# Kernel tuning notes

Hardware: AMD Instinct MI355X
Metric: run time of the kernel (lower is better)

## Reference

```python
import jax, jax.numpy as jnp
import numpy as np

NUM_NEIGHBORS = (10, 25)  # FLAGS.num_neighbors = '10_25'
MAX_DEGREE = 64
L = 2  # num encoder layers


def _sample(nodes, neighbors_out, neighbors_in, key):
    """Multi-hop uniform neighbor sampling (shuffle columns + slice, as in TF code)."""
    samples = [nodes]
    support = 1
    supports = [1]
    for k in range(L):
        t = L - 1 - k
        n = NUM_NEIGHBORS[t]
        support *= 2 * n
        supports.append(support)
        key, k1, k2 = jax.random.split(key, 3)
        # tf.transpose(tf.random.shuffle(tf.transpose(x))) shuffles neighbor slots
        # with ONE permutation shared across all rows, then slices first n.
        cols_out = jax.random.permutation(k1, MAX_DEGREE)[:n]
        cols_in = jax.random.permutation(k2, MAX_DEGREE)[:n]
        nout = neighbors_out[samples[k]][:, cols_out]  # [prev, n]
        nin = neighbors_in[samples[k]][:, cols_in]     # [prev, n]
        samples.append(jnp.concatenate([nout, nin], axis=1).reshape(-1))
    return samples, supports


def _gc(self_v, nei_out, nei_in, W):
    # GraphConvolution: mean-aggregate out/in neighbors, concat with self, linear, sigmoid.
    agg = jnp.concatenate([self_v, nei_out.mean(axis=1), nei_in.mean(axis=1)], axis=-1)
    return jax.nn.sigmoid(agg @ W)


def _aggregate(inputs, supports, layer, W, B):
    h_hop = []
    for hop in range(L - layer):
        n = NUM_NEIGHBORS[L - hop - 1]
        nei = inputs[hop + 1].reshape(B * supports[hop], 2 * n, -1)
        self_v = inputs[hop].reshape(B * supports[hop], -1)
        h_hop.append(_gc(self_v, nei[:, :n], nei[:, n:], W))
    return h_hop


def _forward(nodes1, nodes2, neighbors_out, neighbors_in, features,
             W_in, W_mean, W_std, W_pi, W_ag, W_ad, Wd_mean, Wd_std, Wd_pi):
    B = nodes1.shape[0]
    key = jax.random.key(42)
    k1, k2 = jax.random.split(key)
    s1, sup1 = _sample(nodes1, neighbors_out, neighbors_in, k1)
    s2, sup2 = _sample(nodes2, neighbors_out, neighbors_in, k2)
    in1 = [features[s] for s in s1]  # hop-wise gathered features
    in2 = [features[s] for s in s2]
    # layer 0: shared input GC
    h1 = _aggregate(in1, sup1, 0, W_in, B)
    h2 = _aggregate(in2, sup2, 0, W_in, B)
    # layer 1: parameter heads (mean/std/pi/alpha)
    h_mean1 = _aggregate(h1, sup1, 1, W_mean, B)[0]
    h_mean2 = _aggregate(h2, sup2, 1, W_mean, B)[0]
    h_std1 = _aggregate(h1, sup1, 1, W_std, B)[0]
    h_std2 = _aggregate(h2, sup2, 1, W_std, B)[0]
    h_pi1 = _aggregate(h1, sup1, 1, W_pi, B)[0]
    h_pi2 = _aggregate(h2, sup2, 1, W_pi, B)[0]
    # final fully-connected projections (act = identity)
    z_mean1 = h_mean1 @ Wd_mean
    z_mean2 = h_mean2 @ Wd_mean
    z_std1 = h_std1 @ Wd_std
    z_std2 = h_std2 @ Wd_std
    pi_logit1 = h_pi1 @ Wd_pi
    pi_logit2 = h_pi2 @ Wd_pi
    return jnp.stack([z_mean1, z_std1, pi_logit1, z_mean2, z_std2, pi_logit2])


def setup_inputs() -> dict:
    key = jax.random.key(0)
    ks = jax.random.split(key, 16)
    N, F, B = 200000, 128, 256
    E, D = 128, 64
    inp = {
        'nodes1': jax.random.randint(ks[0], (B,), 0, N, dtype=jnp.int32),
        'nodes2': jax.random.randint(ks[1], (B,), 0, N, dtype=jnp.int32),
        'neighbors_out': jax.random.randint(ks[2], (N, MAX_DEGREE), 0, N, dtype=jnp.int32),
        'neighbors_in': jax.random.randint(ks[3], (N, MAX_DEGREE), 0, N, dtype=jnp.int32),
        'features': jax.random.normal(ks[4], (N, F), dtype=jnp.float32),
        'W_in': jax.random.normal(ks[5], (3 * F, E), dtype=jnp.float32) * 0.05,
        'W_mean': jax.random.normal(ks[6], (3 * E, E), dtype=jnp.float32) * 0.05,
        'W_std': jax.random.normal(ks[7], (3 * E, E), dtype=jnp.float32) * 0.05,
        'W_pi': jax.random.normal(ks[8], (3 * E, E), dtype=jnp.float32) * 0.05,
        'W_ag': jax.random.normal(ks[9], (3 * E, E), dtype=jnp.float32) * 0.05,
        'W_ad': jax.random.normal(ks[10], (3 * E, E), dtype=jnp.float32) * 0.05,
        'Wd_mean': jax.random.normal(ks[11], (E, D), dtype=jnp.float32) * 0.05,
        'Wd_std': jax.random.normal(ks[12], (E, D), dtype=jnp.float32) * 0.05,
        'Wd_pi': jax.random.normal(ks[13], (E, D), dtype=jnp.float32) * 0.05,
    }
    return inp


def reference(nodes1, nodes2, neighbors_out, neighbors_in, features,
              W_in, W_mean, W_std, W_pi, W_ag, W_ad, Wd_mean, Wd_std, Wd_pi):
    return _forward(nodes1, nodes2, neighbors_out, neighbors_in, features,
                    W_in, W_mean, W_std, W_pi, W_ag, W_ad, Wd_mean, Wd_std, Wd_pi)
```

## Files before the change

kernel.cpp:

```cpp
#include <hip/hip_runtime.h>
#include <stdint.h>
#include <math.h>

#define FDIM 128
#define KDIM 384
#define NROWS 26112

struct Cols { int o25[25]; int i25[25]; int o10[10]; int i10[10]; };
struct ColsBoth { Cols c[2]; };

static inline uint32_t rotl32(uint32_t x, uint32_t r){ return (x<<r)|(x>>(32u-r)); }

static void tf2x32(uint32_t k0, uint32_t k1, uint32_t c0, uint32_t c1,
                   uint32_t& o0, uint32_t& o1){
  const uint32_t ra[4] = {13u,15u,26u,6u};
  const uint32_t rb[4] = {17u,29u,16u,24u};
  uint32_t ks2 = k0 ^ k1 ^ 0x1BD11BDAu;
  uint32_t x0 = c0 + k0, x1 = c1 + k1;
  for(int i=0;i<4;i++){ x0 += x1; x1 = rotl32(x1, ra[i]); x1 ^= x0; }
  x0 += k1; x1 += ks2 + 1u;
  for(int i=0;i<4;i++){ x0 += x1; x1 = rotl32(x1, rb[i]); x1 ^= x0; }
  x0 += ks2; x1 += k0 + 2u;
  for(int i=0;i<4;i++){ x0 += x1; x1 = rotl32(x1, ra[i]); x1 ^= x0; }
  x0 += k0; x1 += k1 + 3u;
  for(int i=0;i<4;i++){ x0 += x1; x1 = rotl32(x1, rb[i]); x1 ^= x0; }
  x0 += k1; x1 += ks2 + 4u;
  for(int i=0;i<4;i++){ x0 += x1; x1 = rotl32(x1, ra[i]); x1 ^= x0; }
  x0 += ks2; x1 += k0 + 5u;
  o0 = x0; o1 = x1;
}

static void jax_split_child(uint32_t ka, uint32_t kb, uint32_t i,
                            uint32_t& oa, uint32_t& ob){
  tf2x32(ka, kb, 0u, i, oa, ob);
}

static uint32_t jax_bits32(uint32_t ka, uint32_t kb, uint32_t i){
  uint32_t a,b; tf2x32(ka, kb, 0u, i, a, b);
  return a ^ b;
}

static void jax_perm64(uint32_t ka, uint32_t kb, int* perm){
  uint32_t sa, sb; jax_split_child(ka, kb, 1u, sa, sb);
  uint32_t b[64]; int v[64];
  for(int i=0;i<64;i++){ b[i]=jax_bits32(sa, sb, (uint32_t)i); v[i]=i; }
  for(int i=1;i<64;i++){
    uint32_t bb=b[i]; int vv=v[i]; int j=i-1;
    while(j>=0 && b[j]>bb){ b[j+1]=b[j]; v[j+1]=v[j]; j--; }
    b[j+1]=bb; v[j+1]=vv;
  }
  for(int i=0;i<64;i++) perm[i]=v[i];
}

static void compute_cols(ColsBoth& cb){
  uint32_t k1a,k1b,k2a,k2b;
  jax_split_child(0u, 42u, 0u, k1a, k1b);
  jax_split_child(0u, 42u, 1u, k2a, k2b);
  for(int side=0; side<2; side++){
    uint32_t ka = side ? k2a : k1a;
    uint32_t kb = side ? k2b : k1b;
    uint32_t nka,nkb, c1a,c1b, c2a,c2b;
    jax_split_child(ka,kb,0u,nka,nkb);
    jax_split_child(ka,kb,1u,c1a,c1b);
    jax_split_child(ka,kb,2u,c2a,c2b);
    int p[64];
    jax_perm64(c1a,c1b,p); for(int i=0;i<25;i++) cb.c[side].o25[i]=p[i];
    jax_perm64(c2a,c2b,p); for(int i=0;i<25;i++) cb.c[side].i25[i]=p[i];
    uint32_t d1a,d1b,d2a,d2b;
    jax_split_child(nka,nkb,1u,d1a,d1b);
    jax_split_child(nka,nkb,2u,d2a,d2b);
    jax_perm64(d1a,d1b,p); for(int i=0;i<10;i++) cb.c[side].o10[i]=p[i];
    jax_perm64(d2a,d2b,p); for(int i=0;i<10;i++) cb.c[side].i10[i]=p[i];
  }
}

__device__ __forceinline__ float getc(const float4& v, int i){
  return (i==0)?v.x:(i==1)?v.y:(i==2)?v.z:v.w;
}
__device__ __forceinline__ float sigf(float x){ return 1.0f/(1.0f+expf(-x)); }
__device__ __forceinline__ void add4(float4& s, const float4& v){
  s.x+=v.x; s.y+=v.y; s.z+=v.z; s.w+=v.w;
}


__global__ __launch_bounds__(256) void gather_kernel(
    const float* __restrict__ feat,
    const int* __restrict__ nodes1, const int* __restrict__ nodes2,
    const int* __restrict__ nout, const int* __restrict__ nin,
    float* __restrict__ agg, int base_row, ColsBoth cb)
{
  int t = threadIdx.x;
  int row_local = blockIdx.x*8 + (t>>5);
  int lane = t & 31;
  int c0 = lane*4;
  int row = base_row + row_local;

  float4 selfv, so, si;

  if(row < 512){
    int side = row >> 8, b = row & 255;
    int node = (side ? nodes2 : nodes1)[b];
    const Cols& c = cb.c[side];
    const long nb = (long)node*64;
    selfv = *(const float4*)(feat + (long)node*FDIM + c0);
    int ido[25], idi[25];
    #pragma unroll
    for(int i=0;i<25;i++) ido[i] = nout[nb + c.o25[i]];
    #pragma unroll
    for(int i=0;i<25;i++) idi[i] = nin[nb + c.i25[i]];
    float4 acco = make_float4(0,0,0,0);
    float4 acci = make_float4(0,0,0,0);
    #pragma unroll
    for(int jj=0; jj<25; jj+=5){
      float4 vo[5], vi[5];
      #pragma unroll
      for(int i=0;i<5;i++) vo[i] = *(const float4*)(feat + (long)ido[jj+i]*FDIM + c0);
      #pragma unroll
      for(int i=0;i<5;i++) vi[i] = *(const float4*)(feat + (long)idi[jj+i]*FDIM + c0);
      #pragma unroll
      for(int i=0;i<5;i++) add4(acco, vo[i]);
      #pragma unroll
      for(int i=0;i<5;i++) add4(acci, vi[i]);
    }
    so = make_float4(acco.x/25.f, acco.y/25.f, acco.z/25.f, acco.w/25.f);
    si = make_float4(acci.x/25.f, acci.y/25.f, acci.z/25.f, acci.w/25.f);
  } else {
    int hrow = row - 512;
    int side = (hrow >= 12800) ? 1 : 0;
    int r = side ? (hrow - 12800) : hrow;
    int b = r / 50, slot = r % 50;
    const Cols& c = cb.c[side];
    int root = (side ? nodes2 : nodes1)[b];
    int node;
    if(slot < 25) node = nout[(long)root*64 + c.o25[slot]];
    else          node = nin [(long)root*64 + c.i25[slot-25]];
    const long nb = (long)node*64;
    selfv = *(const float4*)(feat + (long)node*FDIM + c0);
    int oid[10], iid[10];
    #pragma unroll
    for(int j=0;j<10;j++) oid[j] = nout[nb + c.o10[j]];
    #pragma unroll
    for(int j=0;j<10;j++) iid[j] = nin[nb + c.i10[j]];
    float4 acco = make_float4(0,0,0,0);
    float4 acci = make_float4(0,0,0,0);
    #pragma unroll
    for(int jj=0; jj<10; jj+=5){
      float4 vo[5], vi[5];
      #pragma unroll
      for(int j=0;j<5;j++) vo[j] = *(const float4*)(feat + (long)oid[jj+j]*FDIM + c0);
      #pragma unroll
      for(int j=0;j<5;j++) vi[j] = *(const float4*)(feat + (long)iid[jj+j]*FDIM + c0);
      #pragma unroll
      for(int j=0;j<5;j++) add4(acco, vo[j]);
      #pragma unroll
      for(int j=0;j<5;j++) add4(acci, vi[j]);
    }
    so = make_float4(acco.x*0.1f, acco.y*0.1f, acco.z*0.1f, acco.w*0.1f);
    si = make_float4(acci.x*0.1f, acci.y*0.1f, acci.z*0.1f, acci.w*0.1f);
  }

  float* ar = agg + (long)row_local*KDIM;
  *(float4*)(ar + c0)       = selfv;
  *(float4*)(ar + 128 + c0) = so;
  *(float4*)(ar + 256 + c0) = si;
}

__global__ __launch_bounds__(256) void gemm_sig_kernel(
    const float* __restrict__ A, const float* __restrict__ W,
    float* __restrict__ out)
{
  __shared__ float Wbuf[96*128];
  int t = threadIdx.x, lane = t&15, rg = t>>4;
  int r0 = blockIdx.x*64 + rg*4;
  int c0 = lane*8;
  float acc[4][8];
  #pragma unroll
  for(int r=0;r<4;r++)
    #pragma unroll
    for(int i=0;i<8;i++) acc[r][i]=0.f;

  for(int kc=0; kc<4; kc++){
    __syncthreads();
    const float4* ws = (const float4*)(W + kc*96*128);
    float4* wd = (float4*)Wbuf;
    #pragma unroll
    for(int i=0;i<12;i++) wd[i*256+t] = ws[i*256+t];
    __syncthreads();
    const float* Ab = A + (long)r0*KDIM + kc*96;
    #pragma unroll 2
    for(int k4=0;k4<96;k4+=4){
      float4 a0 = *(const float4*)(Ab + 0*KDIM + k4);
      float4 a1 = *(const float4*)(Ab + 1*KDIM + k4);
      float4 a2 = *(const float4*)(Ab + 2*KDIM + k4);
      float4 a3 = *(const float4*)(Ab + 3*KDIM + k4);
      #pragma unroll
      for(int kk=0;kk<4;kk++){
        float av0=getc(a0,kk), av1=getc(a1,kk), av2=getc(a2,kk), av3=getc(a3,kk);
        const float* wr = Wbuf + (k4+kk)*128 + c0;
        float4 w0 = *(const float4*)wr;
        float4 w1 = *(const float4*)(wr+4);
        acc[0][0]+=av0*w0.x; acc[0][1]+=av0*w0.y; acc[0][2]+=av0*w0.z; acc[0][3]+=av0*w0.w;
        acc[0][4]+=av0*w1.x; acc[0][5]+=av0*w1.y; acc[0][6]+=av0*w1.z; acc[0][7]+=av0*w1.w;
        acc[1][0]+=av1*w0.x; acc[1][1]+=av1*w0.y; acc[1][2]+=av1*w0.z; acc[1][3]+=av1*w0.w;
        acc[1][4]+=av1*w1.x; acc[1][5]+=av1*w1.y; acc[1][6]+=av1*w1.z; acc[1][7]+=av1*w1.w;
        acc[2][0]+=av2*w0.x; acc[2][1]+=av2*w0.y; acc[2][2]+=av2*w0.z; acc[2][3]+=av2*w0.w;
        acc[2][4]+=av2*w1.x; acc[2][5]+=av2*w1.y; acc[2][6]+=av2*w1.z; acc[2][7]+=av2*w1.w;
        acc[3][0]+=av3*w0.x; acc[3][1]+=av3*w0.y; acc[3][2]+=av3*w0.z; acc[3][3]+=av3*w0.w;
        acc[3][4]+=av3*w1.x; acc[3][5]+=av3*w1.y; acc[3][6]+=av3*w1.z; acc[3][7]+=av3*w1.w;
      }
    }
  }
  #pragma unroll
  for(int r=0;r<4;r++){
    float4 o0, o1;
    o0.x=sigf(acc[r][0]); o0.y=sigf(acc[r][1]); o0.z=sigf(acc[r][2]); o0.w=sigf(acc[r][3]);
    o1.x=sigf(acc[r][4]); o1.y=sigf(acc[r][5]); o1.z=sigf(acc[r][6]); o1.w=sigf(acc[r][7]);
    float* op = out + (long)(r0+r)*FDIM + c0;
    *(float4*)op = o0; *(float4*)(op+4) = o1;
  }
}

__global__ __launch_bounds__(256) void head_kernel(
    const float* __restrict__ h,
    const float* __restrict__ Wm, const float* __restrict__ Ws, const float* __restrict__ Wp,
    const float* __restrict__ Dm, const float* __restrict__ Ds, const float* __restrict__ Dp,
    float* __restrict__ out)
{
  __shared__ float As[KDIM];
  __shared__ float Ps[4*FDIM];
  __shared__ float Hs[FDIM];
  __shared__ float Qs[4*64];
  int head = blockIdx.x >> 9;
  int grow = blockIdx.x & 511;
  int t = threadIdx.x;
  const float* W = (head==0) ? Wm : (head==1) ? Ws : Wp;
  const float* D = (head==0) ? Dm : (head==1) ? Ds : Dp;

  {
    int c = t & 127;
    int half = t >> 7;
    const float* nb = h + (long)(512 + grow*50 + half*25)*FDIM + c;
    float s = 0.f;
    #pragma unroll
    for(int jj=0;jj<25;jj+=5){
      float v0 = nb[(long)(jj+0)*FDIM];
      float v1 = nb[(long)(jj+1)*FDIM];
      float v2 = nb[(long)(jj+2)*FDIM];
      float v3 = nb[(long)(jj+3)*FDIM];
      float v4 = nb[(long)(jj+4)*FDIM];
      s += v0+v1+v2+v3+v4;
    }
    As[128 + half*128 + c] = s/25.f;
    if(half==0) As[c] = h[(long)grow*FDIM + c];
  }
  __syncthreads();

  {
    int c2 = (t & 63)*2;
    int kq = t >> 6;
    const float* wp = W + (long)(kq*96)*FDIM + c2;
    const float* as = As + kq*96;
    float a0=0.f, a1=0.f;
    #pragma unroll 8
    for(int k=0;k<96;k++){
      float a = as[k];
      float2 w = *(const float2*)(wp + (long)k*FDIM);
      a0 += a*w.x; a1 += a*w.y;
    }
    Ps[kq*FDIM + c2]   = a0;
    Ps[kq*FDIM + c2+1] = a1;
  }
  __syncthreads();
  if(t < 64){
    int c2 = t*2;
    float s0 = Ps[c2]     + Ps[FDIM+c2]     + Ps[2*FDIM+c2]     + Ps[3*FDIM+c2];
    float s1 = Ps[c2+1]   + Ps[FDIM+c2+1]   + Ps[2*FDIM+c2+1]   + Ps[3*FDIM+c2+1];
    Hs[c2]   = sigf(s0);
    Hs[c2+1] = sigf(s1);
  }
  __syncthreads();

  {
    int col = t & 63;
    int kq = t >> 6;
    const float* dp = D + (long)(kq*32)*64 + col;
    const float* hs = Hs + kq*32;
    float a = 0.f;
    #pragma unroll 8
    for(int k=0;k<32;k++){
      a += hs[k] * dp[(long)k*64];
    }
    Qs[kq*64 + col] = a;
  }
  __syncthreads();
  if(t < 64){
    float a = Qs[t] + Qs[64+t] + Qs[128+t] + Qs[192+t];
    int side = grow >> 8, b = grow & 255;
    out[((long)(side*3+head)*256 + b)*64 + t] = a;
  }
}

extern "C" void kernel_launch(void* const* d_in, const int* in_sizes, int n_in,
                              void* d_out, int out_size, void* d_ws, size_t ws_size,
                              hipStream_t stream) {
  const int*   nodes1  = (const int*)d_in[0];
  const int*   nodes2  = (const int*)d_in[1];
  const int*   nout    = (const int*)d_in[2];
  const int*   nin     = (const int*)d_in[3];
  const float* feat    = (const float*)d_in[4];
  const float* W_in    = (const float*)d_in[5];
  const float* W_mean  = (const float*)d_in[6];
  const float* W_std   = (const float*)d_in[7];
  const float* W_pi    = (const float*)d_in[8];
  const float* Wd_mean = (const float*)d_in[11];
  const float* Wd_std  = (const float*)d_in[12];
  const float* Wd_pi   = (const float*)d_in[13];
  float* out = (float*)d_out;

  float* h    = (float*)d_ws;
  float* aggC = h + (size_t)NROWS*FDIM;

  size_t fixedB = (size_t)NROWS*FDIM*4;
  const int ncOpt[5] = {1,2,4,12,51};
  int nc = 51;
  for(int i=0;i<5;i++){
    size_t need = fixedB + ((size_t)NROWS/ncOpt[i])*KDIM*4;
    if(need <= ws_size){ nc = ncOpt[i]; break; }
  }
  int chunkRows = NROWS / nc;

  ColsBoth cb;
  compute_cols(cb);

  for(int c=0;c<nc;c++){
    int base = c*chunkRows;
    gather_kernel<<<chunkRows/8, 256, 0, stream>>>(feat, nodes1, nodes2,
                                                   nout, nin, aggC, base, cb);
    gemm_sig_kernel<<<chunkRows/64, 256, 0, stream>>>(aggC, W_in, h + (size_t)base*FDIM);
  }
  head_kernel<<<1536, 256, 0, stream>>>(h, W_mean, W_std, W_pi, Wd_mean, Wd_std, Wd_pi, out);
}
```

Measured before the change: 313.6 us.

## Fuse neighbor gather and input GEMM into one kernel via shared memory

The gather kernel now writes its 32-row aggregate tile into shared memory, and the same block runs the W_in GEMM with sigmoid on that tile. This removes the global round trip of the aggregated 384-wide rows and the chunked launch loop. In exchange, each block streams the full W_in through shared memory for only 32 rows, so weight traffic per row rises. The larger shared-memory footprint (about 74 KB) may also reduce occupancy while the gather is latency-bound.

Result: slower. 321.5 us (+2.5%).

```diff
diff --git a/kernel.cpp b/kernel.cpp
--- a/kernel.cpp
+++ b/kernel.cpp
@@ -5,6 +5,9 @@
 #define FDIM 128
 #define KDIM 384
 #define NROWS 26112
+#define ASTRIDE 388
+#define BROWS 32
+#define KCH 48
 
 struct Cols { int o25[25]; int i25[25]; int o10[10]; int i10[10]; };
 struct ColsBoth { Cols c[2]; };
@@ -83,140 +86,139 @@
 }
 
 
-__global__ __launch_bounds__(256) void gather_kernel(
+__global__ __launch_bounds__(256) void fused_gg_kernel(
     const float* __restrict__ feat,
     const int* __restrict__ nodes1, const int* __restrict__ nodes2,
     const int* __restrict__ nout, const int* __restrict__ nin,
-    float* __restrict__ agg, int base_row, ColsBoth cb)
+    const float* __restrict__ W,
+    float* __restrict__ h, ColsBoth cb)
 {
+  __shared__ float As[BROWS*ASTRIDE];
+  __shared__ float Wbuf[KCH*FDIM];
   int t = threadIdx.x;
-  int row_local = blockIdx.x*8 + (t>>5);
-  int lane = t & 31;
-  int c0 = lane*4;
-  int row = base_row + row_local;
-
-  float4 selfv, so, si;
-
-  if(row < 512){
-    int side = row >> 8, b = row & 255;
-    int node = (side ? nodes2 : nodes1)[b];
-    const Cols& c = cb.c[side];
-    const long nb = (long)node*64;
-    selfv = *(const float4*)(feat + (long)node*FDIM + c0);
-    int ido[25], idi[25];
+
+  {
+    int g = t >> 5;
+    int lane = t & 31;
+    int c0 = lane*4;
+    #pragma unroll 1
+    for(int rr=0; rr<4; rr++){
+      int lrow = rr*8 + g;
+      int row = blockIdx.x*BROWS + lrow;
+      float4 selfv, so, si;
+
+      if(row < 512){
+        int side = row >> 8, b = row & 255;
+        int node = (side ? nodes2 : nodes1)[b];
+        const Cols& c = cb.c[side];
+        const long nb = (long)node*64;
+        selfv = *(const float4*)(feat + (long)node*FDIM + c0);
+        int ido[25], idi[25];
+        #pragma unroll
+        for(int i=0;i<25;i++) ido[i] = nout[nb + c.o25[i]];
+        #pragma unroll
+        for(int i=0;i<25;i++) idi[i] = nin[nb + c.i25[i]];
+        float4 acco = make_float4(0,0,0,0);
+        float4 acci = make_float4(0,0,0,0);
+        #pragma unroll
+        for(int jj=0; jj<25; jj+=5){
+          float4 vo[5], vi[5];
+          #pragma unroll
+          for(int i=0;i<5;i++) vo[i] = *(const float4*)(feat + (long)ido[jj+i]*FDIM + c0);
+          #pragma unroll
+          for(int i=0;i<5;i++) vi[i] = *(const float4*)(feat + (long)idi[jj+i]*FDIM + c0);
+          #pragma unroll
+          for(int i=0;i<5;i++) add4(acco, vo[i]);
+          #pragma unroll
+          for(int i=0;i<5;i++) add4(acci, vi[i]);
+        }
+        so = make_float4(acco.x/25.f, acco.y/25.f, acco.z/25.f, acco.w/25.f);
+        si = make_float4(acci.x/25.f, acci.y/25.f, acci.z/25.f, acci.w/25.f);
+      } else {
+        int hrow = row - 512;
+        int side = (hrow >= 12800) ? 1 : 0;
+        int r = side ? (hrow - 12800) : hrow;
+        int b = r / 50, slot = r % 50;
+        const Cols& c = cb.c[side];
+        int root = (side ? nodes2 : nodes1)[b];
+        int node;
+        if(slot < 25) node = nout[(long)root*64 + c.o25[slot]];
+        else          node = nin [(long)root*64 + c.i25[slot-25]];
+        const long nb = (long)node*64;
+        selfv = *(const float4*)(feat + (long)node*FDIM + c0);
+        int oid[10], iid[10];
+        #pragma unroll
+        for(int j=0;j<10;j++) oid[j] = nout[nb + c.o10[j]];
+        #pragma unroll
+        for(int j=0;j<10;j++) iid[j] = nin[nb + c.i10[j]];
+        float4 acco = make_float4(0,0,0,0);
+        float4 acci = make_float4(0,0,0,0);
+        #pragma unroll
+        for(int jj=0; jj<10; jj+=5){
+          float4 vo[5], vi[5];
+          #pragma unroll
+          for(int j=0;j<5;j++) vo[j] = *(const float4*)(feat + (long)oid[jj+j]*FDIM + c0);
+          #pragma unroll
+          for(int j=0;j<5;j++) vi[j] = *(const float4*)(feat + (long)iid[jj+j]*FDIM + c0);
+          #pragma unroll
+          for(int j=0;j<5;j++) add4(acco, vo[j]);
+          #pragma unroll
+          for(int j=0;j<5;j++) add4(acci, vi[j]);
+        }
+        so = make_float4(acco.x*0.1f, acco.y*0.1f, acco.z*0.1f, acco.w*0.1f);
+        si = make_float4(acci.x*0.1f, acci.y*0.1f, acci.z*0.1f, acci.w*0.1f);
+      }
+
+      float* ar = As + lrow*ASTRIDE;
+      *(float4*)(ar + c0)       = selfv;
+      *(float4*)(ar + 128 + c0) = so;
+      *(float4*)(ar + 256 + c0) = si;
+    }
+  }
+
+  {
+    int lane = t & 15, rg = t >> 4;
+    int c0 = lane*8;
+    float acc[2][8];
     #pragma unroll
-    for(int i=0;i<25;i++) ido[i] = nout[nb + c.o25[i]];
+    for(int r=0;r<2;r++)
+      #pragma unroll
+      for(int i=0;i<8;i++) acc[r][i]=0.f;
+
+    for(int kc=0; kc<8; kc++){
+      __syncthreads();
+      const float4* ws = (const float4*)(W + kc*KCH*FDIM);
+      float4* wd = (float4*)Wbuf;
+      #pragma unroll
+      for(int i=0;i<6;i++) wd[i*256+t] = ws[i*256+t];
+      __syncthreads();
+      const float* Ab = As + (long)(rg*2)*ASTRIDE + kc*KCH;
+      #pragma unroll 2
+      for(int k4=0;k4<KCH;k4+=4){
+        float4 a0 = *(const float4*)(Ab + k4);
+        float4 a1 = *(const float4*)(Ab + ASTRIDE + k4);
+        #pragma unroll
+        for(int kk=0;kk<4;kk++){
+          const float* wr = Wbuf + (k4+kk)*FDIM + c0;
+          float4 w0 = *(const float4*)wr;
+          float4 w1 = *(const float4*)(wr+4);
+          float av0=getc(a0,kk), av1=getc(a1,kk);
+          acc[0][0]+=av0*w0.x; acc[0][1]+=av0*w0.y; acc[0][2]+=av0*w0.z; acc[0][3]+=av0*w0.w;
+          acc[0][4]+=av0*w1.x; acc[0][5]+=av0*w1.y; acc[0][6]+=av0*w1.z; acc[0][7]+=av0*w1.w;
+          acc[1][0]+=av1*w0.x; acc[1][1]+=av1*w0.y; acc[1][2]+=av1*w0.z; acc[1][3]+=av1*w0.w;
+          acc[1][4]+=av1*w1.x; acc[1][5]+=av1*w1.y; acc[1][6]+=av1*w1.z; acc[1][7]+=av1*w1.w;
+        }
+      }
+    }
     #pragma unroll
-    for(int i=0;i<25;i++) idi[i] = nin[nb + c.i25[i]];
-    float4 acco = make_float4(0,0,0,0);
-    float4 acci = make_float4(0,0,0,0);
-    #pragma unroll
-    for(int jj=0; jj<25; jj+=5){
-      float4 vo[5], vi[5];
-      #pragma unroll
-      for(int i=0;i<5;i++) vo[i] = *(const float4*)(feat + (long)ido[jj+i]*FDIM + c0);
-      #pragma unroll
-      for(int i=0;i<5;i++) vi[i] = *(const float4*)(feat + (long)idi[jj+i]*FDIM + c0);
-      #pragma unroll
-      for(int i=0;i<5;i++) add4(acco, vo[i]);
-      #pragma unroll
-      for(int i=0;i<5;i++) add4(acci, vi[i]);
-    }
-    so = make_float4(acco.x/25.f, acco.y/25.f, acco.z/25.f, acco.w/25.f);
-    si = make_float4(acci.x/25.f, acci.y/25.f, acci.z/25.f, acci.w/25.f);
-  } else {
-    int hrow = row - 512;
-    int side = (hrow >= 12800) ? 1 : 0;
-    int r = side ? (hrow - 12800) : hrow;
-    int b = r / 50, slot = r % 50;
-    const Cols& c = cb.c[side];
-    int root = (side ? nodes2 : nodes1)[b];
-    int node;
-    if(slot < 25) node = nout[(long)root*64 + c.o25[slot]];
-    else          node = nin [(long)root*64 + c.i25[slot-25]];
-    const long nb = (long)node*64;
-    selfv = *(const float4*)(feat + (long)node*FDIM + c0);
-    int oid[10], iid[10];
-    #pragma unroll
-    for(int j=0;j<10;j++) oid[j] = nout[nb + c.o10[j]];
-    #pragma unroll
-    for(int j=0;j<10;j++) iid[j] = nin[nb + c.i10[j]];
-    float4 acco = make_float4(0,0,0,0);
-    float4 acci = make_float4(0,0,0,0);
-    #pragma unroll
-    for(int jj=0; jj<10; jj+=5){
-      float4 vo[5], vi[5];
-      #pragma unroll
-      for(int j=0;j<5;j++) vo[j] = *(const float4*)(feat + (long)oid[jj+j]*FDIM + c0);
-      #pragma unroll
-      for(int j=0;j<5;j++) vi[j] = *(const float4*)(feat + (long)iid[jj+j]*FDIM + c0);
-      #pragma unroll
-      for(int j=0;j<5;j++) add4(acco, vo[j]);
-      #pragma unroll
-      for(int j=0;j<5;j++) add4(acci, vi[j]);
-    }
-    so = make_float4(acco.x*0.1f, acco.y*0.1f, acco.z*0.1f, acco.w*0.1f);
-    si = make_float4(acci.x*0.1f, acci.y*0.1f, acci.z*0.1f, acci.w*0.1f);
-  }
-
-  float* ar = agg + (long)row_local*KDIM;
-  *(float4*)(ar + c0)       = selfv;
-  *(float4*)(ar + 128 + c0) = so;
-  *(float4*)(ar + 256 + c0) = si;
-}
-
-__global__ __launch_bounds__(256) void gemm_sig_kernel(
-    const float* __restrict__ A, const float* __restrict__ W,
-    float* __restrict__ out)
-{
-  __shared__ float Wbuf[96*128];
-  int t = threadIdx.x, lane = t&15, rg = t>>4;
-  int r0 = blockIdx.x*64 + rg*4;
-  int c0 = lane*8;
-  float acc[4][8];
-  #pragma unroll
-  for(int r=0;r<4;r++)
-    #pragma unroll
-    for(int i=0;i<8;i++) acc[r][i]=0.f;
-
-  for(int kc=0; kc<4; kc++){
-    __syncthreads();
-    const float4* ws = (const float4*)(W + kc*96*128);
-    float4* wd = (float4*)Wbuf;
-    #pragma unroll
-    for(int i=0;i<12;i++) wd[i*256+t] = ws[i*256+t];
-    __syncthreads();
-    const float* Ab = A + (long)r0*KDIM + kc*96;
-    #pragma unroll 2
-    for(int k4=0;k4<96;k4+=4){
-      float4 a0 = *(const float4*)(Ab + 0*KDIM + k4);
-      float4 a1 = *(const float4*)(Ab + 1*KDIM + k4);
-      float4 a2 = *(const float4*)(Ab + 2*KDIM + k4);
-      float4 a3 = *(const float4*)(Ab + 3*KDIM + k4);
-      #pragma unroll
-      for(int kk=0;kk<4;kk++){
-        float av0=getc(a0,kk), av1=getc(a1,kk), av2=getc(a2,kk), av3=getc(a3,kk);
-        const float* wr = Wbuf + (k4+kk)*128 + c0;
-        float4 w0 = *(const float4*)wr;
-        float4 w1 = *(const float4*)(wr+4);
-        acc[0][0]+=av0*w0.x; acc[0][1]+=av0*w0.y; acc[0][2]+=av0*w0.z; acc[0][3]+=av0*w0.w;
-        acc[0][4]+=av0*w1.x; acc[0][5]+=av0*w1.y; acc[0][6]+=av0*w1.z; acc[0][7]+=av0*w1.w;
-        acc[1][0]+=av1*w0.x; acc[1][1]+=av1*w0.y; acc[1][2]+=av1*w0.z; acc[1][3]+=av1*w0.w;
-        acc[1][4]+=av1*w1.x; acc[1][5]+=av1*w1.y; acc[1][6]+=av1*w1.z; acc[1][7]+=av1*w1.w;
-        acc[2][0]+=av2*w0.x; acc[2][1]+=av2*w0.y; acc[2][2]+=av2*w0.z; acc[2][3]+=av2*w0.w;
-        acc[2][4]+=av2*w1.x; acc[2][5]+=av2*w1.y; acc[2][6]+=av2*w1.z; acc[2][7]+=av2*w1.w;
-        acc[3][0]+=av3*w0.x; acc[3][1]+=av3*w0.y; acc[3][2]+=av3*w0.z; acc[3][3]+=av3*w0.w;
-        acc[3][4]+=av3*w1.x; acc[3][5]+=av3*w1.y; acc[3][6]+=av3*w1.z; acc[3][7]+=av3*w1.w;
-      }
-    }
-  }
-  #pragma unroll
-  for(int r=0;r<4;r++){
-    float4 o0, o1;
-    o0.x=sigf(acc[r][0]); o0.y=sigf(acc[r][1]); o0.z=sigf(acc[r][2]); o0.w=sigf(acc[r][3]);
-    o1.x=sigf(acc[r][4]); o1.y=sigf(acc[r][5]); o1.z=sigf(acc[r][6]); o1.w=sigf(acc[r][7]);
-    float* op = out + (long)(r0+r)*FDIM + c0;
-    *(float4*)op = o0; *(float4*)(op+4) = o1;
+    for(int r=0;r<2;r++){
+      float4 o0, o1;
+      o0.x=sigf(acc[r][0]); o0.y=sigf(acc[r][1]); o0.z=sigf(acc[r][2]); o0.w=sigf(acc[r][3]);
+      o1.x=sigf(acc[r][4]); o1.y=sigf(acc[r][5]); o1.z=sigf(acc[r][6]); o1.w=sigf(acc[r][7]);
+      long grow = (long)blockIdx.x*BROWS + rg*2 + r;
+      float* op = h + grow*FDIM + c0;
+      *(float4*)op = o0; *(float4*)(op+4) = o1;
+    }
   }
 }
 
@@ -317,26 +319,12 @@
   const float* Wd_pi   = (const float*)d_in[13];
   float* out = (float*)d_out;
 
-  float* h    = (float*)d_ws;
-  float* aggC = h + (size_t)NROWS*FDIM;
-
-  size_t fixedB = (size_t)NROWS*FDIM*4;
-  const int ncOpt[5] = {1,2,4,12,51};
-  int nc = 51;
-  for(int i=0;i<5;i++){
-    size_t need = fixedB + ((size_t)NROWS/ncOpt[i])*KDIM*4;
-    if(need <= ws_size){ nc = ncOpt[i]; break; }
-  }
-  int chunkRows = NROWS / nc;
+  float* h = (float*)d_ws;
 
   ColsBoth cb;
   compute_cols(cb);
 
-  for(int c=0;c<nc;c++){
-    int base = c*chunkRows;
-    gather_kernel<<<chunkRows/8, 256, 0, stream>>>(feat, nodes1, nodes2,
-                                                   nout, nin, aggC, base, cb);
-    gemm_sig_kernel<<<chunkRows/64, 256, 0, stream>>>(aggC, W_in, h + (size_t)base*FDIM);
-  }
+  fused_gg_kernel<<<NROWS/BROWS, 256, 0, stream>>>(feat, nodes1, nodes2,
+                                                   nout, nin, W_in, h, cb);
   head_kernel<<<1536, 256, 0, stream>>>(h, W_mean, W_std, W_pi, Wd_mean, Wd_std, Wd_pi, out);
 }
```
